# Performance work log

Measured on AMD Instinct MI355X. Metric: run time of the kernel, lower is better.

## Reference

```python
import jax, jax.numpy as jnp
import numpy as np
from jax import lax

DN = ('NCDHW', 'OIDHW', 'NCDHW')

def _reflect_conv(s, w, pad_dhw):
    # s: [B,2,D,H,W]; reflect-pad spatial dims then VALID conv -> same spatial size
    p = jnp.pad(s, ((0, 0), (0, 0)) + pad_dhw, mode='reflect')
    return lax.conv_general_dilated(p, w, window_strides=(1, 1, 1),
                                    padding='VALID', dimension_numbers=DN)

def setup_inputs() -> dict:
    key = jax.random.key(0)
    k = jax.random.split(key, 5)
    x = jax.random.normal(k[0], (4, 32, 16, 128, 128), dtype=jnp.float32)
    w1 = jax.random.normal(k[1], (1, 2, 7, 7, 5), dtype=jnp.float32) * 0.1
    w2 = jax.random.normal(k[2], (1, 2, 5, 5, 3), dtype=jnp.float32) * 0.1
    w3 = jax.random.normal(k[3], (1, 2, 3, 3, 1), dtype=jnp.float32) * 0.2
    wf = jax.random.normal(k[4], (1, 3, 1, 1, 1), dtype=jnp.float32) * 0.5
    return {'x': x, 'w1': w1, 'w2': w2, 'w3': w3, 'wf': wf}

def reference(x, w1, w2, w3, wf):
    # channel pool: mean & max over channel dim -> [B,2,D,H,W]
    s_in = jnp.concatenate([jnp.mean(x, axis=1, keepdims=True),
                            jnp.max(x, axis=1, keepdims=True)], axis=1)
    # branch pads in (D,H,W) order match kernels (7,7,5)/(5,5,3)/(3,3,1)
    s1 = _reflect_conv(s_in, w1, ((3, 3), (3, 3), (2, 2)))
    s2 = _reflect_conv(s_in, w2, ((2, 2), (2, 2), (1, 1)))
    s3 = _reflect_conv(s_in, w3, ((1, 1), (1, 1), (0, 0)))
    s = jnp.concatenate([s1, s2, s3], axis=1)  # [B,3,D,H,W]
    fused = lax.conv_general_dilated(s, wf, window_strides=(1, 1, 1),
                                     padding='VALID', dimension_numbers=DN)
    spatial_weight = jax.nn.sigmoid(fused)  # [B,1,D,H,W]
    return x * spatial_weight
```

## Files before the change

### kernel.cpp

```cpp
#include <hip/hip_runtime.h>
#include <math.h>

#define B_ 4
#define C_ 32
#define D_ 16
#define H_ 128
#define W_ 128
#define HW_ (H_*W_)
#define SP_ (D_*HW_)

#define PW_ 136
#define PPL_ (H_*PW_)
#define PCH_ (D_*PPL_)

typedef float f32x4 __attribute__((ext_vector_type(4)));
typedef float f32x4u __attribute__((ext_vector_type(4), aligned(4)));

__device__ __forceinline__ int refl(int i, int n) {
    i = (i < 0) ? -i : i;
    i = (i >= n) ? (2*n - 2 - i) : i;
    return i;
}

__device__ __forceinline__ void prep_one(int t, const float* __restrict__ w1,
                                         const float* __restrict__ w2,
                                         const float* __restrict__ w3,
                                         const float* __restrict__ wf,
                                         float* __restrict__ Wc) {
    int ow = t % 5;
    int oh = (t / 5) % 7;
    int od = (t / 35) % 7;
    int ci = t / 245;
    float v = wf[0] * w1[((ci*7+od)*7+oh)*5+ow];
    if (od>=1 && od<=5 && oh>=1 && oh<=5 && ow>=1 && ow<=3)
        v = fmaf(wf[1], w2[((ci*5+(od-1))*5+(oh-1))*3+(ow-1)], v);
    if (od>=2 && od<=4 && oh>=2 && oh<=4 && ow==2)
        v = fmaf(wf[2], w3[(ci*3+(od-2))*3+(oh-2)], v);
    Wc[t] = v;
}

__global__ __launch_bounds__(256) void pool_kernel(
        const float* __restrict__ x, float* __restrict__ s,
        const float* __restrict__ w1, const float* __restrict__ w2,
        const float* __restrict__ w3, const float* __restrict__ wf,
        float* __restrict__ Wc, int b0) {
    if (blockIdx.x >= 512) {
        int t = threadIdx.x;
        if (t < 245) prep_one(t, w1, w2, w3, wf, Wc);
        int t2 = t + 245;
        if (t2 < 490) prep_one(t2, w1, w2, w3, wf, Wc);
        return;
    }
    int idx = blockIdx.x * 256 + threadIdx.x;
    int w4 = (idx & 31) * 4;
    int rest = idx >> 5;
    int h = rest & 127;
    int bd = rest >> 7;
    int d = bd & 15;
    int b = b0 + (bd >> 4);
    const float* xp = x + (b*C_*D_ + d)*HW_ + h*W_ + w4;
    f32x4 v = *(const f32x4*)xp;
    f32x4 sm = v, mx = v;
    #pragma unroll 8
    for (int c = 1; c < C_; ++c) {
        f32x4 u = *(const f32x4*)(xp + c*SP_);
        sm += u;
        mx.x=fmaxf(mx.x,u.x); mx.y=fmaxf(mx.y,u.y);
        mx.z=fmaxf(mx.z,u.z); mx.w=fmaxf(mx.w,u.w);
    }
    sm *= (1.0f/32.0f);
    float* rm = s + (b*2+0)*PCH_ + d*PPL_ + h*PW_;
    float* rM = s + (b*2+1)*PCH_ + d*PPL_ + h*PW_;
    *(f32x4u*)(rm + w4 + 2) = sm;
    *(f32x4u*)(rM + w4 + 2) = mx;
    if (w4 == 0) {
        rm[0] = sm.z; rm[1] = sm.y;
        rM[0] = mx.z; rM[1] = mx.y;
    } else if (w4 == 124) {
        rm[130] = sm.z; rm[131] = sm.y;
        rM[130] = mx.z; rM[131] = mx.y;
    }
}

__global__ __launch_bounds__(256, 2) void spatial_att_kernel(
        const float* __restrict__ x,
        const float* __restrict__ s,
        const float* __restrict__ Wc,
        float* __restrict__ out, int b0) {
    int bid = blockIdx.x;
    int ht = bid & 15;
    int dp = (bid >> 4) & 7;
    int b  = b0 + (bid >> 7);
    int t = threadIdx.x;
    int w0 = (t & 31) * 4;
    int h0 = ht * 8 + (t >> 5);
    int d0 = dp * 2;

    int drow[8];
    #pragma unroll
    for (int k = 0; k < 8; ++k) drow[k] = refl(d0 + k - 3, D_) * PPL_;

    float acc0[4] = {0.f, 0.f, 0.f, 0.f};
    float acc1[4] = {0.f, 0.f, 0.f, 0.f};

    for (int ci = 0; ci < 2; ++ci) {
        const float* sc = s + (b*2 + ci)*PCH_;
        const float* wcb_ci = Wc + ci*245;
        for (int oh = 0; oh < 7; ++oh) {
            const float* sh = sc + refl(h0 + oh - 3, H_)*PW_ + w0;
            const float* wcb = wcb_ci + oh*5;
            #pragma unroll
            for (int k = 0; k < 8; ++k) {
                const float* rp = sh + drow[k];
                const f32x4 L = *(const f32x4*)(rp);
                const f32x4 R = *(const f32x4*)(rp + 4);
                float v[8] = {L.x, L.y, L.z, L.w, R.x, R.y, R.z, R.w};
                if (k <= 6) {
                    const float* wp = wcb + k*35;
                    #pragma unroll
                    for (int ow = 0; ow < 5; ++ow) {
                        float wgt = wp[ow];
                        #pragma unroll
                        for (int wi = 0; wi < 4; ++wi)
                            acc0[wi] = fmaf(wgt, v[wi+ow], acc0[wi]);
                    }
                }
                if (k >= 1) {
                    const float* wp = wcb + (k-1)*35;
                    #pragma unroll
                    for (int ow = 0; ow < 5; ++ow) {
                        float wgt = wp[ow];
                        #pragma unroll
                        for (int wi = 0; wi < 4; ++wi)
                            acc1[wi] = fmaf(wgt, v[wi+ow], acc1[wi]);
                    }
                }
            }
        }
    }

    float sg0[4], sg1[4];
    #pragma unroll
    for (int wi = 0; wi < 4; ++wi) {
        sg0[wi] = 1.0f/(1.0f + __expf(-acc0[wi]));
        sg1[wi] = 1.0f/(1.0f + __expf(-acc1[wi]));
    }

    int obase = (b*C_*D_ + d0)*HW_ + h0*W_ + w0;
    #pragma unroll 8
    for (int c = 0; c < C_; ++c) {
        int i0 = obase + c*SP_;
        f32x4 xv0 = *(const f32x4*)(x + i0);
        f32x4 xv1 = *(const f32x4*)(x + i0 + HW_);
        f32x4 o0; o0.x=xv0.x*sg0[0]; o0.y=xv0.y*sg0[1]; o0.z=xv0.z*sg0[2]; o0.w=xv0.w*sg0[3];
        f32x4 o1; o1.x=xv1.x*sg1[0]; o1.y=xv1.y*sg1[1]; o1.z=xv1.z*sg1[2]; o1.w=xv1.w*sg1[3];
        *(f32x4*)(out + i0) = o0;
        *(f32x4*)(out + i0 + HW_) = o1;
    }
}

extern "C" void kernel_launch(void* const* d_in, const int* in_sizes, int n_in,
                              void* d_out, int out_size, void* d_ws, size_t ws_size,
                              hipStream_t stream) {
    const float* x  = (const float*)d_in[0];
    const float* w1 = (const float*)d_in[1];
    const float* w2 = (const float*)d_in[2];
    const float* w3 = (const float*)d_in[3];
    const float* wf = (const float*)d_in[4];
    float* out = (float*)d_out;
    float* Wc = (float*)d_ws;
    float* s  = (float*)d_ws + 512;

    pool_kernel<<<513, 256, 0, stream>>>(x, s, w1, w2, w3, wf, Wc, 0);
    spatial_att_kernel<<<256, 256, 0, stream>>>(x, s, Wc, out, 0);
    pool_kernel<<<512, 256, 0, stream>>>(x, s, w1, w2, w3, wf, Wc, 2);
    spatial_att_kernel<<<256, 256, 0, stream>>>(x, s, Wc, out, 2);
}
```

Before: 92.74 us.

## Process all batches in single pool and attention launches with one depth per thread

Replaces the two half-batch pool and attention launch pairs with one pool launch and one attention launch covering all four batches. Each attention thread now computes one depth slice instead of two adjacent ones, which doubles the block count and raises the occupancy hint from 2 to 4. This cuts launch overhead and the register pressure of the two-accumulator loop. In exchange it drops the reuse of shared depth rows between adjacent slices. It also gives up the half-batch split that let the second read of x likely hit in the large last-level cache, since the full x tensor is far bigger than a half-batch slice.

```diff
diff --git a/kernel.cpp b/kernel.cpp
--- a/kernel.cpp
+++ b/kernel.cpp
@@ -43,8 +43,8 @@
         const float* __restrict__ x, float* __restrict__ s,
         const float* __restrict__ w1, const float* __restrict__ w2,
         const float* __restrict__ w3, const float* __restrict__ wf,
-        float* __restrict__ Wc, int b0) {
-    if (blockIdx.x >= 512) {
+        float* __restrict__ Wc) {
+    if (blockIdx.x >= 1024) {
         int t = threadIdx.x;
         if (t < 245) prep_one(t, w1, w2, w3, wf, Wc);
         int t2 = t + 245;
@@ -57,7 +57,7 @@
     int h = rest & 127;
     int bd = rest >> 7;
     int d = bd & 15;
-    int b = b0 + (bd >> 4);
+    int b = bd >> 4;
     const float* xp = x + (b*C_*D_ + d)*HW_ + h*W_ + w4;
     f32x4 v = *(const f32x4*)xp;
     f32x4 sm = v, mx = v;
@@ -82,26 +82,24 @@
     }
 }
 
-__global__ __launch_bounds__(256, 2) void spatial_att_kernel(
+__global__ __launch_bounds__(256, 4) void spatial_att_kernel(
         const float* __restrict__ x,
         const float* __restrict__ s,
         const float* __restrict__ Wc,
-        float* __restrict__ out, int b0) {
+        float* __restrict__ out) {
     int bid = blockIdx.x;
     int ht = bid & 15;
-    int dp = (bid >> 4) & 7;
-    int b  = b0 + (bid >> 7);
+    int d0 = (bid >> 4) & 15;
+    int b  = bid >> 8;
     int t = threadIdx.x;
     int w0 = (t & 31) * 4;
     int h0 = ht * 8 + (t >> 5);
-    int d0 = dp * 2;
 
-    int drow[8];
+    int drow[7];
     #pragma unroll
-    for (int k = 0; k < 8; ++k) drow[k] = refl(d0 + k - 3, D_) * PPL_;
+    for (int k = 0; k < 7; ++k) drow[k] = refl(d0 + k - 3, D_) * PPL_;
 
-    float acc0[4] = {0.f, 0.f, 0.f, 0.f};
-    float acc1[4] = {0.f, 0.f, 0.f, 0.f};
+    float acc[4] = {0.f, 0.f, 0.f, 0.f};
 
     for (int ci = 0; ci < 2; ++ci) {
         const float* sc = s + (b*2 + ci)*PCH_;
@@ -110,52 +108,35 @@
             const float* sh = sc + refl(h0 + oh - 3, H_)*PW_ + w0;
             const float* wcb = wcb_ci + oh*5;
             #pragma unroll
-            for (int k = 0; k < 8; ++k) {
+            for (int k = 0; k < 7; ++k) {
                 const float* rp = sh + drow[k];
                 const f32x4 L = *(const f32x4*)(rp);
                 const f32x4 R = *(const f32x4*)(rp + 4);
                 float v[8] = {L.x, L.y, L.z, L.w, R.x, R.y, R.z, R.w};
-                if (k <= 6) {
-                    const float* wp = wcb + k*35;
+                const float* wp = wcb + k*35;
+                #pragma unroll
+                for (int ow = 0; ow < 5; ++ow) {
+                    float wgt = wp[ow];
                     #pragma unroll
-                    for (int ow = 0; ow < 5; ++ow) {
-                        float wgt = wp[ow];
-                        #pragma unroll
-                        for (int wi = 0; wi < 4; ++wi)
-                            acc0[wi] = fmaf(wgt, v[wi+ow], acc0[wi]);
-                    }
-                }
-                if (k >= 1) {
-                    const float* wp = wcb + (k-1)*35;
-                    #pragma unroll
-                    for (int ow = 0; ow < 5; ++ow) {
-                        float wgt = wp[ow];
-                        #pragma unroll
-                        for (int wi = 0; wi < 4; ++wi)
-                            acc1[wi] = fmaf(wgt, v[wi+ow], acc1[wi]);
-                    }
+                    for (int wi = 0; wi < 4; ++wi)
+                        acc[wi] = fmaf(wgt, v[wi+ow], acc[wi]);
                 }
             }
         }
     }
 
-    float sg0[4], sg1[4];
+    float sg[4];
     #pragma unroll
-    for (int wi = 0; wi < 4; ++wi) {
-        sg0[wi] = 1.0f/(1.0f + __expf(-acc0[wi]));
-        sg1[wi] = 1.0f/(1.0f + __expf(-acc1[wi]));
-    }
+    for (int wi = 0; wi < 4; ++wi)
+        sg[wi] = 1.0f/(1.0f + __expf(-acc[wi]));
 
     int obase = (b*C_*D_ + d0)*HW_ + h0*W_ + w0;
     #pragma unroll 8
     for (int c = 0; c < C_; ++c) {
         int i0 = obase + c*SP_;
-        f32x4 xv0 = *(const f32x4*)(x + i0);
-        f32x4 xv1 = *(const f32x4*)(x + i0 + HW_);
-        f32x4 o0; o0.x=xv0.x*sg0[0]; o0.y=xv0.y*sg0[1]; o0.z=xv0.z*sg0[2]; o0.w=xv0.w*sg0[3];
-        f32x4 o1; o1.x=xv1.x*sg1[0]; o1.y=xv1.y*sg1[1]; o1.z=xv1.z*sg1[2]; o1.w=xv1.w*sg1[3];
-        *(f32x4*)(out + i0) = o0;
-        *(f32x4*)(out + i0 + HW_) = o1;
+        f32x4 xv = *(const f32x4*)(x + i0);
+        f32x4 o; o.x=xv.x*sg[0]; o.y=xv.y*sg[1]; o.z=xv.z*sg[2]; o.w=xv.w*sg[3];
+        *(f32x4*)(out + i0) = o;
     }
 }
 
@@ -171,8 +152,6 @@
     float* Wc = (float*)d_ws;
     float* s  = (float*)d_ws + 512;
 
-    pool_kernel<<<513, 256, 0, stream>>>(x, s, w1, w2, w3, wf, Wc, 0);
-    spatial_att_kernel<<<256, 256, 0, stream>>>(x, s, Wc, out, 0);
-    pool_kernel<<<512, 256, 0, stream>>>(x, s, w1, w2, w3, wf, Wc, 2);
-    spatial_att_kernel<<<256, 256, 0, stream>>>(x, s, Wc, out, 2);
+    pool_kernel<<<1025, 256, 0, stream>>>(x, s, w1, w2, w3, wf, Wc);
+    spatial_att_kernel<<<B_*D_*(H_/8), 256, 0, stream>>>(x, s, Wc, out);
 }
```

Result: faster. 85.15 us (-8.2%).
